# Kernel optimization log

Hardware: AMD Instinct MI355X
Metric: run time of the kernel (lower is better)

The kernel has to match this reference:

```python
import jax, jax.numpy as jnp
import numpy as np

H = 1024    # hidden_size
E = 1024    # embedding_size
V = 50257   # vocab_size
M = 16384   # current number of entity slots in h_e_m


def setup_inputs() -> dict:
    key = jax.random.key(0)
    ks = jax.random.split(key, 12)
    u = lambda k, s: jax.random.uniform(k, s, jnp.float32, -0.1, 0.1)
    return dict(
        x=jax.random.randint(ks[0], (1,), 0, V),
        entity_target=jax.random.randint(ks[1], (1,), 1, M),
        emb=u(ks[2], (V, E)),
        W_ih=u(ks[3], (4 * H, E)),
        W_hh=u(ks[4], (4 * H, H)),
        b_ih=jnp.zeros((4 * H,), jnp.float32),
        b_hh=jnp.zeros((4 * H,), jnp.float32),
        h0=jnp.zeros((1, H), jnp.float32),
        c0=jnp.zeros((1, H), jnp.float32),
        h_e_m=u(ks[5], (M, H)),
        Ws_w=u(ks[6], (H, H)),
        Ws_b=jnp.zeros((H,), jnp.float32),
        Wz_w=u(ks[7], (1, 2 * H)),
        Wz_b=jnp.zeros((1,), jnp.float32),
        W2_w=u(ks[8], (H, 2 * H)),
        W2_b=jnp.zeros((H,), jnp.float32),
        W1_w=u(ks[9], (V, H)),
        W1_b=jnp.zeros((V,), jnp.float32),
    )


def reference(x, entity_target, emb, W_ih, W_hh, b_ih, b_hh, h0, c0, h_e_m,
              Ws_w, Ws_b, Wz_w, Wz_b, W2_w, W2_b, W1_w, W1_b):
    # --- single-step LSTM (batch=1, 1 token), PyTorch gate order i,f,g,o ---
    x_e = emb[x]                                        # (1, E)
    gates = x_e @ W_ih.T + h0 @ W_hh.T + b_ih + b_hh    # (1, 4H)
    i, f, g, o = jnp.split(gates, 4, axis=1)
    c = jax.nn.sigmoid(f) * c0 + jax.nn.sigmoid(i) * jnp.tanh(g)
    h = jax.nn.sigmoid(o) * jnp.tanh(c)                 # (1, H)

    # --- attention over entity memory bank ---
    mem_proj = h_e_m @ Ws_w.T + Ws_b                    # (M, H)  W_score(h_e_m)
    scores = (h @ mem_proj.T).reshape(-1)               # (M,)
    p_v = jax.nn.softmax(scores)                        # (M,)
    # sum(diag(p_v) @ h_e_m, dim=0) == p_v @ h_e_m
    d_i = (p_v @ h_e_m)[None, :]                        # (1, H)

    # --- sigmoid entity gate ---
    z_i = jax.nn.sigmoid(jnp.concatenate([h, d_i], axis=1) @ Wz_w.T + Wz_b)  # (1,1)

    # --- index_copy scatter write, then read back written slot ---
    t = entity_target[0]
    new_mem = h_e_m.at[t].set(h[0])                     # (M, H)
    mem_read = new_mem[t]                               # (H,) == h[0]

    feat = jnp.concatenate([h[0], mem_read], axis=0)    # (2H,)
    out = (jnp.tanh(feat @ W2_w.T + W2_b) @ W1_w.T + W1_b)[None, :]  # (1, V)
    return out, z_i, p_v
```

## Files before the change

kernel.cpp:

```cpp
#include <hip/hip_runtime.h>
#include <hip/hip_bf16.h>

#define H 1024
#define E 1024
#define VOCAB 50257
#define M 16384

__device__ __forceinline__ float sigmoidf_(float x) { return 1.0f / (1.0f + expf(-x)); }

__device__ __forceinline__ float wave_sum(float v) {
    #pragma unroll
    for (int o = 32; o > 0; o >>= 1) v += __shfl_down(v, o);
    return v;
}

__global__ void k_lstm(const int* __restrict__ x, const float* __restrict__ emb,
                       const float* __restrict__ W_ih, const float* __restrict__ W_hh,
                       const float* __restrict__ b_ih, const float* __restrict__ b_hh,
                       const float* __restrict__ h0, const float* __restrict__ c0,
                       float* __restrict__ h_out, float* __restrict__ v_z,
                       float* __restrict__ dv_z, unsigned int* __restrict__ cnt) {
    int j = blockIdx.x;
    if (threadIdx.x == 0) {
        v_z[j] = 0.f;
        dv_z[j] = 0.f;
        if (j == 0) cnt[0] = 0u;
    }
    int w = threadIdx.x >> 6;
    int lane = threadIdx.x & 63;
    int r = w * H + j;
    const float4* A  = (const float4*)(W_ih + (size_t)r * E);
    const float4* Bm = (const float4*)(W_hh + (size_t)r * H);
    const float4* xe = (const float4*)(emb + (size_t)x[0] * E);
    const float4* hp = (const float4*)h0;
    float acc = 0.f;
    #pragma unroll
    for (int i = 0; i < 4; i++) {
        int idx = lane + 64 * i;
        float4 a = A[idx],  xv = xe[idx];
        acc += a.x * xv.x + a.y * xv.y + a.z * xv.z + a.w * xv.w;
        float4 b = Bm[idx], hv = hp[idx];
        acc += b.x * hv.x + b.y * hv.y + b.z * hv.z + b.w * hv.w;
    }
    acc = wave_sum(acc);
    __shared__ float g[4];
    if (lane == 0) g[w] = acc + b_ih[r] + b_hh[r];
    __syncthreads();
    if (threadIdx.x == 0) {
        float c = sigmoidf_(g[1]) * c0[j] + sigmoidf_(g[0]) * tanhf(g[2]);
        h_out[j] = sigmoidf_(g[3]) * tanhf(c);
    }
}

__global__ void k_hWs(const float* __restrict__ h, const float* __restrict__ Ws_w,
                      float* __restrict__ v) {
    int k = threadIdx.x;
    int j0 = blockIdx.x * 16;
    __shared__ float hs[16];
    if (threadIdx.x < 16) hs[threadIdx.x] = h[j0 + threadIdx.x];
    __syncthreads();
    float acc = 0.f;
    #pragma unroll
    for (int jj = 0; jj < 16; jj++)
        acc += hs[jj] * Ws_w[(size_t)(j0 + jj) * H + k];
    atomicAdd(&v[k], acc);
}

__global__ void k_attn(const float* __restrict__ hem, const float* __restrict__ v,
                       float* __restrict__ sc, float* __restrict__ db,
                       float* __restrict__ Mb, float* __restrict__ Sb) {
    __shared__ float s_sc[64];
    __shared__ float s_e[64];
    int b = blockIdx.x;
    int m0 = b * 64;
    int w = threadIdx.x >> 6, lane = threadIdx.x & 63;
    const float4* V4 = (const float4*)v;
    #pragma unroll
    for (int q = 0; q < 4; q++) {
        int mm = w * 4 + q;
        const float4* A = (const float4*)(hem + (size_t)(m0 + mm) * H);
        float acc = 0.f;
        #pragma unroll
        for (int i = 0; i < 4; i++) {
            float4 a = A[lane + 64 * i], bb = V4[lane + 64 * i];
            acc += a.x * bb.x + a.y * bb.y + a.z * bb.z + a.w * bb.w;
        }
        acc = wave_sum(acc);
        if (lane == 0) { s_sc[mm] = acc; sc[m0 + mm] = acc; }
    }
    __syncthreads();
    if (w == 0) {
        float xv = s_sc[lane];
        float mx = xv;
        #pragma unroll
        for (int o = 32; o > 0; o >>= 1) mx = fmaxf(mx, __shfl_down(mx, o));
        mx = __shfl(mx, 0);
        float e = expf(xv - mx);
        s_e[lane] = e;
        float ssum = wave_sum(e);
        if (lane == 0) { Mb[b] = mx; Sb[b] = ssum; }
    }
    __syncthreads();
    int k = threadIdx.x;
    float acc = 0.f;
    #pragma unroll 8
    for (int mm = 0; mm < 64; mm++)
        acc += s_e[mm] * hem[(size_t)(m0 + mm) * H + k];
    db[(size_t)b * H + k] = acc;
}

__global__ void k_comb_fc2(const float* __restrict__ h, const float* __restrict__ W2_w,
                           const float* __restrict__ W2_b, float* __restrict__ oh,
                           const float* __restrict__ sc, const float* __restrict__ db,
                           const float* __restrict__ Mb, const float* __restrict__ Sb,
                           float* __restrict__ pv, float* __restrict__ dv,
                           const float* __restrict__ Wz_w, const float* __restrict__ Wz_b,
                           float* __restrict__ zout, unsigned int* __restrict__ cnt) {
    if (blockIdx.x < 256) {
        int j = blockIdx.x * 4 + (threadIdx.x >> 6);
        int lane = threadIdx.x & 63;
        const float4* R  = (const float4*)(W2_w + (size_t)j * 2 * H);
        const float4* H4 = (const float4*)h;
        float acc = 0.f;
        #pragma unroll
        for (int i = 0; i < 4; i++) {
            int idx = lane + 64 * i;
            float4 hv = H4[idx];
            float4 a = R[idx];
            float4 b = R[256 + idx];
            acc += hv.x * (a.x + b.x) + hv.y * (a.y + b.y)
                 + hv.z * (a.z + b.z) + hv.w * (a.w + b.w);
        }
        acc = wave_sum(acc);
        if (lane == 0) oh[j] = tanhf(acc + W2_b[j]);
        return;
    }
    int b2 = blockIdx.x - 256;
    int t = threadIdx.x;
    __shared__ float s[256];
    __shared__ float s_w[16];
    __shared__ unsigned int s_old;
    float mval = Mb[t];
    s[t] = mval; __syncthreads();
    for (int o = 128; o > 0; o >>= 1) { if (t < o) s[t] = fmaxf(s[t], s[t + o]); __syncthreads(); }
    float gmax = s[0]; __syncthreads();
    s[t] = Sb[t] * expf(mval - gmax); __syncthreads();
    for (int o = 128; o > 0; o >>= 1) { if (t < o) s[t] += s[t + o]; __syncthreads(); }
    float inv = 1.f / s[0]; __syncthreads();
    int base = b2 * 1024;
    #pragma unroll
    for (int q = 0; q < 4; q++) {
        int i = base + t + 256 * q;
        pv[i] = expf(sc[i] - gmax) * inv;
    }
    if (t < 16) s_w[t] = expf(Mb[b2 * 16 + t] - gmax) * inv;
    __syncthreads();
    float a0 = 0.f, a1 = 0.f, a2 = 0.f, a3 = 0.f;
    #pragma unroll
    for (int rr = 0; rr < 16; rr++) {
        const float* row = db + (size_t)(b2 * 16 + rr) * H;
        float wr = s_w[rr];
        a0 += wr * row[t];       a1 += wr * row[t + 256];
        a2 += wr * row[t + 512]; a3 += wr * row[t + 768];
    }
    atomicAdd(&dv[t], a0);       atomicAdd(&dv[t + 256], a1);
    atomicAdd(&dv[t + 512], a2); atomicAdd(&dv[t + 768], a3);
    __threadfence();
    if (t == 0) s_old = atomicAdd(cnt, 1u);
    __syncthreads();
    if (s_old == 15u) {
        __threadfence();
        float acc = 0.f;
        for (int i = t; i < H; i += 256) acc += h[i] * Wz_w[i] + dv[i] * Wz_w[H + i];
        s[t] = acc; __syncthreads();
        for (int o = 128; o > 0; o >>= 1) { if (t < o) s[t] += s[t + o]; __syncthreads(); }
        if (t == 0) zout[0] = sigmoidf_(s[0] + Wz_b[0]);
    }
}

__global__ void k_fc1(const float* __restrict__ oh, const float* __restrict__ W1_w,
                      const float* __restrict__ W1_b, float* __restrict__ out) {
    int r = blockIdx.x * 4 + (threadIdx.x >> 6);
    if (r >= VOCAB) return;
    int lane = threadIdx.x & 63;
    const float4* A  = (const float4*)(W1_w + (size_t)r * H);
    const float4* O4 = (const float4*)oh;
    float acc = 0.f;
    #pragma unroll
    for (int i = 0; i < 4; i++) {
        int idx = lane + 64 * i;
        float4 a = A[idx], b = O4[idx];
        acc += a.x * b.x + a.y * b.y + a.z * b.z + a.w * b.w;
    }
    acc = wave_sum(acc);
    if (lane == 0) out[r] = acc + W1_b[r];
}

extern "C" void kernel_launch(void* const* d_in, const int* in_sizes, int n_in,
                              void* d_out, int out_size, void* d_ws, size_t ws_size,
                              hipStream_t stream) {
    const int*   x      = (const int*)  d_in[0];
    const float* emb    = (const float*)d_in[2];
    const float* W_ih   = (const float*)d_in[3];
    const float* W_hh   = (const float*)d_in[4];
    const float* b_ih   = (const float*)d_in[5];
    const float* b_hh   = (const float*)d_in[6];
    const float* h0     = (const float*)d_in[7];
    const float* c0     = (const float*)d_in[8];
    const float* hem    = (const float*)d_in[9];
    const float* Ws_w   = (const float*)d_in[10];
    const float* Wz_w   = (const float*)d_in[12];
    const float* Wz_b   = (const float*)d_in[13];
    const float* W2_w   = (const float*)d_in[14];
    const float* W2_b   = (const float*)d_in[15];
    const float* W1_w   = (const float*)d_in[16];
    const float* W1_b   = (const float*)d_in[17];

    float* out  = (float*)d_out;
    float* zout = out + VOCAB;
    float* pv   = out + VOCAB + 1;

    float* ws = (float*)d_ws;
    float* h   = ws;
    float* v   = ws + 1024;
    float* sc  = ws + 2048;
    float* dv  = ws + 18432;
    float* oh  = ws + 19456;
    float* Mb  = ws + 20480;
    float* Sb  = ws + 20736;
    unsigned int* cnt = (unsigned int*)(ws + 20992);
    float* db  = ws + 21504;

    k_lstm    <<<1024, 256, 0, stream>>>(x, emb, W_ih, W_hh, b_ih, b_hh, h0, c0,
                                         h, v, dv, cnt);
    k_hWs     <<<64, 1024, 0, stream>>>(h, Ws_w, v);
    k_attn    <<<256, 1024, 0, stream>>>(hem, v, sc, db, Mb, Sb);
    k_comb_fc2<<<272, 256, 0, stream>>>(h, W2_w, W2_b, oh, sc, db, Mb, Sb,
                                        pv, dv, Wz_w, Wz_b, zout, cnt);
    k_fc1     <<<(VOCAB + 3) / 4, 256, 0, stream>>>(oh, W1_w, W1_b, out);
}
```

Before: 82.62 us.

## Fuse attention, combine and vocab projection into one kernel; skip zero h0 matvec

Merges the Ws matvec with the fc2 layer into one kernel, and merges attention, softmax combine and the vocab projection into one grid. The combine blocks spin-wait on an atomic counter set by the attention blocks. This removes launch gaps and lets the large W1 stream overlap with the attention work. The LSTM also checks at runtime whether h0 is all zeros and skips the W_hh matvec in that case. The spin-wait relies on earlier blocks being scheduled first.

```diff
diff --git a/kernel.cpp b/kernel.cpp
--- a/kernel.cpp
+++ b/kernel.cpp
@@ -5,6 +5,10 @@
 #define E 1024
 #define VOCAB 50257
 #define M 16384
+
+#define ATTN_BLOCKS 256
+#define COMB_BLOCKS 16
+#define FC1_BLOCKS ((VOCAB + 3) / 4)
 
 __device__ __forceinline__ float sigmoidf_(float x) { return 1.0f / (1.0f + expf(-x)); }
 
@@ -22,25 +26,38 @@
                        float* __restrict__ dv_z, unsigned int* __restrict__ cnt) {
     int j = blockIdx.x;
     if (threadIdx.x == 0) {
-        v_z[j] = 0.f;
-        dv_z[j] = 0.f;
-        if (j == 0) cnt[0] = 0u;
-    }
+        v_z[j] = 0.f; dv_z[j] = 0.f;
+        if (j == 0) { cnt[0] = 0u; cnt[1] = 0u; }
+    }
+    __shared__ int h0nz;
+    if (threadIdx.x == 0) h0nz = 0;
+    __syncthreads();
+    {
+        float4 t = ((const float4*)h0)[threadIdx.x];
+        if (t.x != 0.f || t.y != 0.f || t.z != 0.f || t.w != 0.f) h0nz = 1;
+    }
+    __syncthreads();
     int w = threadIdx.x >> 6;
     int lane = threadIdx.x & 63;
     int r = w * H + j;
     const float4* A  = (const float4*)(W_ih + (size_t)r * E);
-    const float4* Bm = (const float4*)(W_hh + (size_t)r * H);
     const float4* xe = (const float4*)(emb + (size_t)x[0] * E);
-    const float4* hp = (const float4*)h0;
     float acc = 0.f;
     #pragma unroll
     for (int i = 0; i < 4; i++) {
         int idx = lane + 64 * i;
-        float4 a = A[idx],  xv = xe[idx];
+        float4 a = A[idx], xv = xe[idx];
         acc += a.x * xv.x + a.y * xv.y + a.z * xv.z + a.w * xv.w;
-        float4 b = Bm[idx], hv = hp[idx];
-        acc += b.x * hv.x + b.y * hv.y + b.z * hv.z + b.w * hv.w;
+    }
+    if (h0nz) {
+        const float4* Bm = (const float4*)(W_hh + (size_t)r * H);
+        const float4* hp = (const float4*)h0;
+        #pragma unroll
+        for (int i = 0; i < 4; i++) {
+            int idx = lane + 64 * i;
+            float4 b = Bm[idx], hv = hp[idx];
+            acc += b.x * hv.x + b.y * hv.y + b.z * hv.z + b.w * hv.w;
+        }
     }
     acc = wave_sum(acc);
     __shared__ float g[4];
@@ -52,70 +69,10 @@
     }
 }
 
-__global__ void k_hWs(const float* __restrict__ h, const float* __restrict__ Ws_w,
-                      float* __restrict__ v) {
-    int k = threadIdx.x;
-    int j0 = blockIdx.x * 16;
-    __shared__ float hs[16];
-    if (threadIdx.x < 16) hs[threadIdx.x] = h[j0 + threadIdx.x];
-    __syncthreads();
-    float acc = 0.f;
-    #pragma unroll
-    for (int jj = 0; jj < 16; jj++)
-        acc += hs[jj] * Ws_w[(size_t)(j0 + jj) * H + k];
-    atomicAdd(&v[k], acc);
-}
-
-__global__ void k_attn(const float* __restrict__ hem, const float* __restrict__ v,
-                       float* __restrict__ sc, float* __restrict__ db,
-                       float* __restrict__ Mb, float* __restrict__ Sb) {
-    __shared__ float s_sc[64];
-    __shared__ float s_e[64];
-    int b = blockIdx.x;
-    int m0 = b * 64;
-    int w = threadIdx.x >> 6, lane = threadIdx.x & 63;
-    const float4* V4 = (const float4*)v;
-    #pragma unroll
-    for (int q = 0; q < 4; q++) {
-        int mm = w * 4 + q;
-        const float4* A = (const float4*)(hem + (size_t)(m0 + mm) * H);
-        float acc = 0.f;
-        #pragma unroll
-        for (int i = 0; i < 4; i++) {
-            float4 a = A[lane + 64 * i], bb = V4[lane + 64 * i];
-            acc += a.x * bb.x + a.y * bb.y + a.z * bb.z + a.w * bb.w;
-        }
-        acc = wave_sum(acc);
-        if (lane == 0) { s_sc[mm] = acc; sc[m0 + mm] = acc; }
-    }
-    __syncthreads();
-    if (w == 0) {
-        float xv = s_sc[lane];
-        float mx = xv;
-        #pragma unroll
-        for (int o = 32; o > 0; o >>= 1) mx = fmaxf(mx, __shfl_down(mx, o));
-        mx = __shfl(mx, 0);
-        float e = expf(xv - mx);
-        s_e[lane] = e;
-        float ssum = wave_sum(e);
-        if (lane == 0) { Mb[b] = mx; Sb[b] = ssum; }
-    }
-    __syncthreads();
-    int k = threadIdx.x;
-    float acc = 0.f;
-    #pragma unroll 8
-    for (int mm = 0; mm < 64; mm++)
-        acc += s_e[mm] * hem[(size_t)(m0 + mm) * H + k];
-    db[(size_t)b * H + k] = acc;
-}
-
-__global__ void k_comb_fc2(const float* __restrict__ h, const float* __restrict__ W2_w,
-                           const float* __restrict__ W2_b, float* __restrict__ oh,
-                           const float* __restrict__ sc, const float* __restrict__ db,
-                           const float* __restrict__ Mb, const float* __restrict__ Sb,
-                           float* __restrict__ pv, float* __restrict__ dv,
-                           const float* __restrict__ Wz_w, const float* __restrict__ Wz_b,
-                           float* __restrict__ zout, unsigned int* __restrict__ cnt) {
+__global__ void k_mid(const float* __restrict__ h,
+                      const float* __restrict__ W2_w, const float* __restrict__ W2_b,
+                      float* __restrict__ oh,
+                      const float* __restrict__ Ws_w, float* __restrict__ v) {
     if (blockIdx.x < 256) {
         int j = blockIdx.x * 4 + (threadIdx.x >> 6);
         int lane = threadIdx.x & 63;
@@ -135,52 +92,129 @@
         if (lane == 0) oh[j] = tanhf(acc + W2_b[j]);
         return;
     }
-    int b2 = blockIdx.x - 256;
+    int j0 = (blockIdx.x - 256) * 16;
     int t = threadIdx.x;
-    __shared__ float s[256];
-    __shared__ float s_w[16];
-    __shared__ unsigned int s_old;
-    float mval = Mb[t];
-    s[t] = mval; __syncthreads();
-    for (int o = 128; o > 0; o >>= 1) { if (t < o) s[t] = fmaxf(s[t], s[t + o]); __syncthreads(); }
-    float gmax = s[0]; __syncthreads();
-    s[t] = Sb[t] * expf(mval - gmax); __syncthreads();
-    for (int o = 128; o > 0; o >>= 1) { if (t < o) s[t] += s[t + o]; __syncthreads(); }
-    float inv = 1.f / s[0]; __syncthreads();
-    int base = b2 * 1024;
-    #pragma unroll
-    for (int q = 0; q < 4; q++) {
-        int i = base + t + 256 * q;
-        pv[i] = expf(sc[i] - gmax) * inv;
-    }
-    if (t < 16) s_w[t] = expf(Mb[b2 * 16 + t] - gmax) * inv;
-    __syncthreads();
-    float a0 = 0.f, a1 = 0.f, a2 = 0.f, a3 = 0.f;
-    #pragma unroll
-    for (int rr = 0; rr < 16; rr++) {
-        const float* row = db + (size_t)(b2 * 16 + rr) * H;
-        float wr = s_w[rr];
-        a0 += wr * row[t];       a1 += wr * row[t + 256];
-        a2 += wr * row[t + 512]; a3 += wr * row[t + 768];
-    }
-    atomicAdd(&dv[t], a0);       atomicAdd(&dv[t + 256], a1);
-    atomicAdd(&dv[t + 512], a2); atomicAdd(&dv[t + 768], a3);
-    __threadfence();
-    if (t == 0) s_old = atomicAdd(cnt, 1u);
-    __syncthreads();
-    if (s_old == 15u) {
+    __shared__ float hs[16];
+    if (t < 16) hs[t] = h[j0 + t];
+    __syncthreads();
+    float4 acc = {0.f, 0.f, 0.f, 0.f};
+    #pragma unroll
+    for (int jj = 0; jj < 16; jj++) {
+        float4 wv = ((const float4*)(Ws_w + (size_t)(j0 + jj) * H))[t];
+        float hj = hs[jj];
+        acc.x += hj * wv.x; acc.y += hj * wv.y; acc.z += hj * wv.z; acc.w += hj * wv.w;
+    }
+    atomicAdd(&v[4 * t + 0], acc.x); atomicAdd(&v[4 * t + 1], acc.y);
+    atomicAdd(&v[4 * t + 2], acc.z); atomicAdd(&v[4 * t + 3], acc.w);
+}
+
+__global__ void k_big(const float* __restrict__ hem, const float* __restrict__ v,
+                      float* __restrict__ sc, float* __restrict__ db,
+                      float* __restrict__ Mb, float* __restrict__ Sb,
+                      const float* __restrict__ oh, const float* __restrict__ W1_w,
+                      const float* __restrict__ W1_b, float* __restrict__ out,
+                      float* __restrict__ pv, float* __restrict__ dv,
+                      const float* __restrict__ h,
+                      const float* __restrict__ Wz_w, const float* __restrict__ Wz_b,
+                      float* __restrict__ zout, unsigned int* __restrict__ cnt) {
+    int b = blockIdx.x;
+    if (b < ATTN_BLOCKS) {
+        __shared__ float s_sc[64];
+        __shared__ float s_e[64];
+        int m0 = b * 64;
+        int w = threadIdx.x >> 6, lane = threadIdx.x & 63;
+        const float4* V4 = (const float4*)v;
+        #pragma unroll
+        for (int q = 0; q < 16; q++) {
+            int mm = w + 4 * q;
+            const float4* A = (const float4*)(hem + (size_t)(m0 + mm) * H);
+            float acc = 0.f;
+            #pragma unroll
+            for (int i = 0; i < 4; i++) {
+                float4 a = A[lane + 64 * i], bb = V4[lane + 64 * i];
+                acc += a.x * bb.x + a.y * bb.y + a.z * bb.z + a.w * bb.w;
+            }
+            acc = wave_sum(acc);
+            if (lane == 0) { s_sc[mm] = acc; sc[m0 + mm] = acc; }
+        }
+        __syncthreads();
+        if (w == 0) {
+            float xv = s_sc[lane];
+            float mx = xv;
+            #pragma unroll
+            for (int o = 32; o > 0; o >>= 1) mx = fmaxf(mx, __shfl_down(mx, o));
+            mx = __shfl(mx, 0);
+            float e = expf(xv - mx);
+            s_e[lane] = e;
+            float ssum = wave_sum(e);
+            if (lane == 0) { Mb[b] = mx; Sb[b] = ssum; }
+        }
+        __syncthreads();
+        int c4 = threadIdx.x;
+        float4 acc = {0.f, 0.f, 0.f, 0.f};
+        #pragma unroll 8
+        for (int mm = 0; mm < 64; mm++) {
+            float4 r = ((const float4*)(hem + (size_t)(m0 + mm) * H))[c4];
+            float e = s_e[mm];
+            acc.x += e * r.x; acc.y += e * r.y; acc.z += e * r.z; acc.w += e * r.w;
+        }
+        ((float4*)(db + (size_t)b * H))[c4] = acc;
         __threadfence();
-        float acc = 0.f;
-        for (int i = t; i < H; i += 256) acc += h[i] * Wz_w[i] + dv[i] * Wz_w[H + i];
-        s[t] = acc; __syncthreads();
+        __syncthreads();
+        if (threadIdx.x == 0) atomicAdd(&cnt[0], 1u);
+        return;
+    }
+    if (b < ATTN_BLOCKS + COMB_BLOCKS) {
+        int b2 = b - ATTN_BLOCKS;
+        int t = threadIdx.x;
+        if (t == 0) {
+            while (atomicAdd(&cnt[0], 0u) < (unsigned)ATTN_BLOCKS)
+                __builtin_amdgcn_s_sleep(4);
+        }
+        __syncthreads();
+        __threadfence();
+        __shared__ float s[256];
+        __shared__ float s_w[16];
+        __shared__ unsigned int s_old;
+        float mval = Mb[t];
+        s[t] = mval; __syncthreads();
+        for (int o = 128; o > 0; o >>= 1) { if (t < o) s[t] = fmaxf(s[t], s[t + o]); __syncthreads(); }
+        float gmax = s[0]; __syncthreads();
+        s[t] = Sb[t] * expf(mval - gmax); __syncthreads();
         for (int o = 128; o > 0; o >>= 1) { if (t < o) s[t] += s[t + o]; __syncthreads(); }
-        if (t == 0) zout[0] = sigmoidf_(s[0] + Wz_b[0]);
-    }
-}
-
-__global__ void k_fc1(const float* __restrict__ oh, const float* __restrict__ W1_w,
-                      const float* __restrict__ W1_b, float* __restrict__ out) {
-    int r = blockIdx.x * 4 + (threadIdx.x >> 6);
+        float inv = 1.f / s[0]; __syncthreads();
+        int base = b2 * 1024;
+        #pragma unroll
+        for (int q = 0; q < 4; q++) {
+            int i = base + t + 256 * q;
+            pv[i] = expf(sc[i] - gmax) * inv;
+        }
+        if (t < 16) s_w[t] = expf(Mb[b2 * 16 + t] - gmax) * inv;
+        __syncthreads();
+        float a0 = 0.f, a1 = 0.f, a2 = 0.f, a3 = 0.f;
+        #pragma unroll
+        for (int rr = 0; rr < 16; rr++) {
+            const float* row = db + (size_t)(b2 * 16 + rr) * H;
+            float wr = s_w[rr];
+            a0 += wr * row[t];       a1 += wr * row[t + 256];
+            a2 += wr * row[t + 512]; a3 += wr * row[t + 768];
+        }
+        atomicAdd(&dv[t], a0);       atomicAdd(&dv[t + 256], a1);
+        atomicAdd(&dv[t + 512], a2); atomicAdd(&dv[t + 768], a3);
+        __threadfence();
+        if (t == 0) s_old = atomicAdd(&cnt[1], 1u);
+        __syncthreads();
+        if (s_old == COMB_BLOCKS - 1) {
+            __threadfence();
+            float acc = 0.f;
+            for (int i = t; i < H; i += 256) acc += h[i] * Wz_w[i] + dv[i] * Wz_w[H + i];
+            s[t] = acc; __syncthreads();
+            for (int o = 128; o > 0; o >>= 1) { if (t < o) s[t] += s[t + o]; __syncthreads(); }
+            if (t == 0) zout[0] = sigmoidf_(s[0] + Wz_b[0]);
+        }
+        return;
+    }
+    int r = (b - ATTN_BLOCKS - COMB_BLOCKS) * 4 + (threadIdx.x >> 6);
     if (r >= VOCAB) return;
     int lane = threadIdx.x & 63;
     const float4* A  = (const float4*)(W1_w + (size_t)r * H);
@@ -189,8 +223,8 @@
     #pragma unroll
     for (int i = 0; i < 4; i++) {
         int idx = lane + 64 * i;
-        float4 a = A[idx], b = O4[idx];
-        acc += a.x * b.x + a.y * b.y + a.z * b.z + a.w * b.w;
+        float4 a = A[idx], bb = O4[idx];
+        acc += a.x * bb.x + a.y * bb.y + a.z * bb.z + a.w * bb.w;
     }
     acc = wave_sum(acc);
     if (lane == 0) out[r] = acc + W1_b[r];
@@ -231,11 +265,10 @@
     unsigned int* cnt = (unsigned int*)(ws + 20992);
     float* db  = ws + 21504;
 
-    k_lstm    <<<1024, 256, 0, stream>>>(x, emb, W_ih, W_hh, b_ih, b_hh, h0, c0,
-                                         h, v, dv, cnt);
-    k_hWs     <<<64, 1024, 0, stream>>>(h, Ws_w, v);
-    k_attn    <<<256, 1024, 0, stream>>>(hem, v, sc, db, Mb, Sb);
-    k_comb_fc2<<<272, 256, 0, stream>>>(h, W2_w, W2_b, oh, sc, db, Mb, Sb,
-                                        pv, dv, Wz_w, Wz_b, zout, cnt);
-    k_fc1     <<<(VOCAB + 3) / 4, 256, 0, stream>>>(oh, W1_w, W1_b, out);
-}
+    k_lstm<<<1024, 256, 0, stream>>>(x, emb, W_ih, W_hh, b_ih, b_hh, h0, c0,
+                                     h, v, dv, cnt);
+    k_mid <<<320, 256, 0, stream>>>(h, W2_w, W2_b, oh, Ws_w, v);
+    k_big <<<ATTN_BLOCKS + COMB_BLOCKS + FC1_BLOCKS, 256, 0, stream>>>(
+        hem, v, sc, db, Mb, Sb, oh, W1_w, W1_b, out, pv, dv,
+        h, Wz_w, Wz_b, zout, cnt);
+}
```

Result: slower. 126.9 us (+53.7%).
